# Optimization experiments

Hardware: AMD Instinct MI355X
Metric: run time of the kernel (lower is better)

## Reference

```python
import jax, jax.numpy as jnp
import numpy as np
from jax import lax

NUM_GROUP = 512
GROUP_SIZE = 32
ENC_CH = 384
BN_EPS = 1e-5


def setup_inputs() -> dict:
    key = jax.random.key(0)
    ks = jax.random.split(key, 8)
    B, N = 16, 8192
    def w(k, o, i):
        return jax.random.normal(k, (o, i), jnp.float32) * (1.0 / np.sqrt(i))
    return {
        "xyz": jax.random.normal(ks[0], (B, N, 3), jnp.float32),
        # first_conv: Conv1d(3,128,1)+BN+ReLU, Conv1d(128,256,1)
        "w1": w(ks[1], 128, 3), "b1": jnp.zeros((128,), jnp.float32),
        "g1": jnp.ones((128,), jnp.float32), "bt1": jnp.zeros((128,), jnp.float32),
        "w2": w(ks[2], 256, 128), "b2": jnp.zeros((256,), jnp.float32),
        # second_conv: Conv1d(512,512,1)+BN+ReLU, Conv1d(512,encoder_channel,1)
        "w3": w(ks[3], 512, 512), "b3": jnp.zeros((512,), jnp.float32),
        "g3": jnp.ones((512,), jnp.float32), "bt3": jnp.zeros((512,), jnp.float32),
        "w4": w(ks[4], ENC_CH, 512), "b4": jnp.zeros((ENC_CH,), jnp.float32),
    }


def fps(xyz, npoint):
    """Farthest point sampling. xyz: [B,N,3] -> indices [B,npoint]."""
    B, N, _ = xyz.shape
    def step(carry, _):
        dist, farthest = carry                       # [B,N], [B]
        centroid = jnp.take_along_axis(xyz, farthest[:, None, None], axis=1)  # [B,1,3]
        d = jnp.sum((xyz - centroid) ** 2, axis=-1)  # [B,N]
        dist = jnp.minimum(dist, d)
        nxt = jnp.argmax(dist, axis=-1)
        return (dist, nxt), farthest
    init = (jnp.full((B, N), 1e10, xyz.dtype), jnp.zeros((B,), jnp.int32))
    _, idxs = lax.scan(step, init, None, length=npoint)
    return idxs.T  # [B,npoint]


def knn_point(nsample, xyz, new_xyz):
    """new_xyz [B,S,3], xyz [B,N,3] -> [B,S,nsample] indices of nearest pts."""
    d = (-2.0 * jnp.einsum('bsc,bnc->bsn', new_xyz, xyz)
         + jnp.sum(new_xyz ** 2, -1)[:, :, None]
         + jnp.sum(xyz ** 2, -1)[:, None, :])
    _, idx = lax.top_k(-d, nsample)
    return idx


def batch_norm(x, gamma, beta):
    # x: [M, L, C]; training-mode BN over (M, L) per channel
    mean = jnp.mean(x, axis=(0, 1), keepdims=True)
    var = jnp.var(x, axis=(0, 1), keepdims=True)
    return (x - mean) * lax.rsqrt(var + BN_EPS) * gamma + beta


def reference(xyz, w1, b1, g1, bt1, w2, b2, w3, b3, g3, bt3, w4, b4):
    B, N, _ = xyz.shape
    G, K = NUM_GROUP, GROUP_SIZE
    # ---- Group: FPS centers + kNN neighborhoods, centered ----
    cidx = fps(xyz, G)                                          # [B,G]
    center = jnp.take_along_axis(xyz, cidx[:, :, None], axis=1) # [B,G,3]
    idx = knn_point(K, xyz, center)                             # [B,G,K]
    nb = jnp.take_along_axis(xyz, idx.reshape(B, G * K, 1), axis=1)
    nb = nb.reshape(B, G, K, 3) - center[:, :, None, :]         # [B,G,K,3]
    # ---- Encoder (PointNet stem), 1x1 conv == channel matmul ----
    pg = nb.reshape(B * G, K, 3)                                # [BG,K,3]
    f = jnp.einsum('mkc,oc->mko', pg, w1) + b1                  # [BG,K,128]
    f = jax.nn.relu(batch_norm(f, g1, bt1))
    f = jnp.einsum('mkc,oc->mko', f, w2) + b2                   # [BG,K,256]
    fg = jnp.max(f, axis=1, keepdims=True)                      # [BG,1,256]
    f = jnp.concatenate([jnp.broadcast_to(fg, f.shape), f], axis=-1)  # [BG,K,512]
    f = jnp.einsum('mkc,oc->mko', f, w3) + b3
    f = jax.nn.relu(batch_norm(f, g3, bt3))
    f = jnp.einsum('mkc,oc->mko', f, w4) + b4                   # [BG,K,C]
    feat = jnp.max(f, axis=1)                                   # [BG,C]
    return feat.reshape(B, G, ENC_CH)
```

## Files before the change

### kernel.cpp

```cpp
#include <hip/hip_runtime.h>
#include <cstddef>

#define B_   16
#define N_   8192
#define G_   512
#define K_   32
#define GT   8192
#define NROW 262144
#define EPS  1e-5f

typedef unsigned short ushort_t;
typedef short bf16x8 __attribute__((ext_vector_type(8)));
typedef float f32x4  __attribute__((ext_vector_type(4)));

constexpr size_t OFF_CENTERS = 0;
constexpr size_t OFF_NB      = OFF_CENTERS + 24576;
constexpr size_t OFF_FG      = OFF_NB      + 786432;
constexpr size_t OFF_C1      = OFF_FG      + 2097152;
constexpr size_t OFF_MOM     = OFF_C1      + 1048576;
constexpr size_t OFF_A       = OFF_MOM     + 16;
constexpr size_t OFF_S1      = OFF_A       + 16384;
constexpr size_t OFF_SF      = OFF_S1      + 128;
constexpr size_t OFF_MU      = OFF_SF      + 256;
constexpr size_t OFF_W2S1    = OFF_MU      + 512;
constexpr size_t OFF_BN1A    = OFF_W2S1    + 256;
constexpr size_t OFF_BN1D    = OFF_BN1A    + 128;
constexpr size_t OFF_BN3A    = OFF_BN1D    + 128;
constexpr size_t OFF_BN3D    = OFF_BN3A    + 512;
constexpr size_t OFF_SFF     = OFF_BN3D    + 512;
constexpr size_t OFF_PFCT    = OFF_SFF     + 65536;
constexpr size_t OFF_T1      = OFF_PFCT    + 32768;
constexpr size_t OFF_SCCW    = OFF_T1      + 32768;
constexpr size_t OFF_SFC     = OFF_SCCW    + 65536;
constexpr size_t OFF_W2T     = OFF_SFC     + 65536;
constexpr size_t OFF_W3T     = OFF_W2T     + 32768;
constexpr size_t OFF_W4H     = OFF_W3T     + 262144;
constexpr size_t OFF_W4L     = OFF_W4H     + 98304;
constexpr size_t OFF_APART   = OFF_W4L     + 98304;
constexpr size_t OFF_W23     = OFF_APART   + 8388608;
constexpr size_t OFF_W23H    = OFF_W23     + 65536;
constexpr size_t OFF_W23L    = OFF_W23H    + 32768;
constexpr size_t OFF_W2H     = OFF_W23L    + 32768;
constexpr size_t OFF_W2L     = OFF_W2H     + 16384;
constexpr size_t WS_FLOATS   = OFF_W2L     + 16384;
constexpr size_t OFF_BASE3   = OFF_APART;

__device__ __forceinline__ unsigned bf16_rne(float v) {
    unsigned u = __float_as_uint(v);
    return (u + 0x7fffu + ((u >> 16) & 1u)) >> 16;
}

__global__ __launch_bounds__(1024) void fps_kernel(const float* __restrict__ xyz,
                                                   float* __restrict__ centers) {
    int b = blockIdx.x, t = threadIdx.x;
    const float* xb = xyz + (size_t)b * N_ * 3;
    float px[8], py[8], pz[8], dist[8];
#pragma unroll
    for (int i = 0; i < 8; ++i) {
        int p = t + (i << 10);
        px[i] = xb[p*3]; py[i] = xb[p*3+1]; pz[i] = xb[p*3+2];
        dist[i] = 1e10f;
    }
    __shared__ float redV[2][16];
    __shared__ int   redI[2][16];
    __shared__ float cxyz[2][3];
    if (t == 0) { cxyz[0][0] = px[0]; cxyz[0][1] = py[0]; cxyz[0][2] = pz[0]; }
    __syncthreads();
    for (int it = 0; it < G_; ++it) {
        int cur = it & 1;
        float lcx = cxyz[cur][0], lcy = cxyz[cur][1], lcz = cxyz[cur][2];
        if (t == 0) {
            float* cd = centers + ((size_t)b * G_ + it) * 3;
            cd[0] = lcx; cd[1] = lcy; cd[2] = lcz;
        }
        float bv = -1.0f; int bp = 0;
#pragma unroll
        for (int i = 0; i < 8; ++i) {
            float dx = __fsub_rn(px[i], lcx);
            float dy = __fsub_rn(py[i], lcy);
            float dz = __fsub_rn(pz[i], lcz);
            float d  = __fadd_rn(__fadd_rn(__fmul_rn(dx,dx), __fmul_rn(dy,dy)), __fmul_rn(dz,dz));
            float nd = fminf(dist[i], d);
            dist[i] = nd;
            if (nd > bv) { bv = nd; bp = t + (i << 10); }
        }
#pragma unroll
        for (int off = 1; off < 64; off <<= 1) {
            float ov = __shfl_xor(bv, off);
            int   op = __shfl_xor(bp, off);
            if (ov > bv || (ov == bv && op < bp)) { bv = ov; bp = op; }
        }
        if ((t & 63) == 0) { redV[cur][t >> 6] = bv; redI[cur][t >> 6] = bp; }
        __syncthreads();
        float v = redV[cur][t & 15]; int p = redI[cur][t & 15];
#pragma unroll
        for (int off = 1; off < 16; off <<= 1) {
            float ov = __shfl_xor(v, off);
            int   op = __shfl_xor(p, off);
            if (ov > v || (ov == v && op < p)) { v = ov; p = op; }
        }
        if ((p & 1023) == t) {
            int i = p >> 10;
            cxyz[cur ^ 1][0] = px[i]; cxyz[cur ^ 1][1] = py[i]; cxyz[cur ^ 1][2] = pz[i];
        }
        __syncthreads();
    }
}

__global__ __launch_bounds__(256) void knn_kernel(const float* __restrict__ xyz,
                                                  const float* __restrict__ centers,
                                                  float* __restrict__ nb) {
    int g = blockIdx.x, t = threadIdx.x;
    int b = g >> 9;
    const float* xb = xyz + (size_t)b * N_ * 3;
    const float* c  = centers + (size_t)g * 3;
    float lcx = c[0], lcy = c[1], lcz = c[2];
    float cn2 = __fadd_rn(__fadd_rn(__fmul_rn(lcx,lcx), __fmul_rn(lcy,lcy)), __fmul_rn(lcz,lcz));
    float dreg[32];
    float bvt = 1e30f; int bpt = 0;
#pragma unroll 8
    for (int i = 0; i < 32; ++i) {
        int p = t + (i << 8);
        float x = xb[p*3], y = xb[p*3+1], z = xb[p*3+2];
        float pn2 = __fadd_rn(__fadd_rn(__fmul_rn(x,x), __fmul_rn(y,y)), __fmul_rn(z,z));
        float dot = __fadd_rn(__fadd_rn(__fmul_rn(lcx,x), __fmul_rn(lcy,y)), __fmul_rn(lcz,z));
        float d   = __fadd_rn(__fadd_rn(__fmul_rn(-2.0f,dot), cn2), pn2);
        dreg[i] = d;
        if (d < bvt) { bvt = d; bpt = p; }
    }
    __shared__ float redV[2][4];
    __shared__ int   redI[2][4];
    int myp = 0;
    for (int s = 0; s < K_; ++s) {
        float bv = bvt; int bp = bpt;
#pragma unroll
        for (int off = 1; off < 64; off <<= 1) {
            float ov = __shfl_xor(bv, off);
            int   op = __shfl_xor(bp, off);
            if (ov < bv || (ov == bv && op < bp)) { bv = ov; bp = op; }
        }
        int buf = s & 1;
        if ((t & 63) == 0) { redV[buf][t >> 6] = bv; redI[buf][t >> 6] = bp; }
        __syncthreads();
        float v = redV[buf][0]; int p = redI[buf][0];
#pragma unroll
        for (int w = 1; w < 4; ++w) {
            float ov = redV[buf][w]; int op = redI[buf][w];
            if (ov < v || (ov == v && op < p)) { v = ov; p = op; }
        }
        if (s == t) myp = p;
        if ((p & 255) == t) {
#pragma unroll
            for (int i = 0; i < 32; ++i)
                if (p == t + (i << 8)) dreg[i] = 1e30f;
            bvt = 1e30f; bpt = t;
#pragma unroll
            for (int i = 0; i < 32; ++i) {
                float vv = dreg[i];
                if (vv < bvt) { bvt = vv; bpt = t + (i << 8); }
            }
        }
    }
    if (t < K_) {
        int p = myp;
        float* dst = nb + ((size_t)g * K_ + t) * 3;
        dst[0] = xb[p*3]   - lcx;
        dst[1] = xb[p*3+1] - lcy;
        dst[2] = xb[p*3+2] - lcz;
    }
}

__global__ void zero_mom_kernel(float* __restrict__ mom) {
    if (threadIdx.x < 16) mom[threadIdx.x] = 0.0f;
}

__global__ void moments_kernel(const float* __restrict__ nb, float* __restrict__ mom) {
    int idx = blockIdx.x * 256 + threadIdx.x;
    float x = nb[idx*3], y = nb[idx*3+1], z = nb[idx*3+2];
    float v[9] = {x, y, z, x*x, y*y, z*z, x*y, x*z, y*z};
    __shared__ float red[4][9];
    int t = threadIdx.x;
#pragma unroll
    for (int q = 0; q < 9; ++q) {
        float s = v[q];
#pragma unroll
        for (int off = 32; off; off >>= 1) s += __shfl_xor(s, off);
        if ((t & 63) == 0) red[t >> 6][q] = s;
    }
    __syncthreads();
    if (t < 9) atomicAdd(&mom[t], red[0][t] + red[1][t] + red[2][t] + red[3][t]);
}

__global__ void bn1_params_kernel(const float* __restrict__ mom,
                                  const float* __restrict__ w1, const float* __restrict__ b1,
                                  const float* __restrict__ g1, const float* __restrict__ bt1,
                                  float* __restrict__ bn1a, float* __restrict__ bn1d) {
    int c = threadIdx.x;
    const float inv_n = 1.0f / (float)NROW;
    float mx = mom[0]*inv_n, my = mom[1]*inv_n, mz = mom[2]*inv_n;
    float cxx = mom[3]*inv_n - mx*mx, cyy = mom[4]*inv_n - my*my, czz = mom[5]*inv_n - mz*mz;
    float cxy = mom[6]*inv_n - mx*my, cxz = mom[7]*inv_n - mx*mz, cyz = mom[8]*inv_n - my*mz;
    float wx = w1[c*3], wy = w1[c*3+1], wz = w1[c*3+2];
    float mean = wx*mx + wy*my + wz*mz + b1[c];
    float var  = wx*wx*cxx + wy*wy*cyy + wz*wz*czz
               + 2.0f*(wx*wy*cxy + wx*wz*cxz + wy*wz*cyz);
    float a = rsqrtf(var + EPS) * g1[c];
    bn1a[c] = a;
    bn1d[c] = (b1[c] - mean) * a + bt1[c];
}

__global__ void transpose_kernel(float* __restrict__ out, const float* __restrict__ in, int R, int C) {
    int t = blockIdx.x * blockDim.x + threadIdx.x;
    if (t < R * C) {
        int i = t / C, j = t % C;
        out[(size_t)j * R + i] = in[t];
    }
}

__global__ void split_kernel(const float* __restrict__ src, ushort_t* __restrict__ hi,
                             ushort_t* __restrict__ lo, int n) {
    int i = blockIdx.x * 256 + threadIdx.x;
    if (i < n) {
        float v = src[i];
        unsigned h = bf16_rne(v);
        hi[i] = (ushort_t)h;
        float r = v - __uint_as_float(h << 16);
        lo[i] = (ushort_t)bf16_rne(r);
    }
}

__global__ __launch_bounds__(256) void p1_mfma_kernel(
        const float* __restrict__ nbg, const float* __restrict__ w1,
        const float* __restrict__ bn1a, const float* __restrict__ bn1d,
        const ushort_t* __restrict__ w2h, const ushort_t* __restrict__ w2l,
        const float* __restrict__ b2,
        float* __restrict__ fg, float* __restrict__ c1,
        float* __restrict__ apart) {
    __shared__ short f1h[32*128], f1l[32*128];
    __shared__ short f1Th[128*40], f1Tl[128*40];
    __shared__ float c1part[2][128];
    __shared__ float nbs[96];
    int t = threadIdx.x;
    int lane = t & 63, w = t >> 6;
    int l15 = lane & 15, lh = lane >> 4;

    f32x4 accA[2][8];
#pragma unroll
    for (int i2 = 0; i2 < 2; ++i2)
#pragma unroll
        for (int j = 0; j < 8; ++j) accA[i2][j] = (f32x4){0.f, 0.f, 0.f, 0.f};

    for (int gi = 0; gi < 16; ++gi) {
        int g = blockIdx.x * 16 + gi;
        if (gi == 0 && t < 96) nbs[t] = nbg[(size_t)g * 96 + t];
        __syncthreads();
        {
            int ch = t & 127, rh = t >> 7;
            float a = bn1a[ch], d = bn1d[ch];
            float w0 = w1[ch*3], wa = w1[ch*3+1], wb = w1[ch*3+2];
            float csum = 0.f;
#pragma unroll
            for (int rr = 0; rr < 16; rr += 2) {
                int r0 = rh*16 + rr;
                unsigned hp[2], lp[2];
#pragma unroll
                for (int u = 0; u < 2; ++u) {
                    int r = r0 + u;
                    float x = nbs[r*3], y = nbs[r*3+1], z = nbs[r*3+2];
                    float m = __fmul_rn(x, w0);
                    m = __fmaf_rn(y, wa, m);
                    m = __fmaf_rn(z, wb, m);
                    m = __fmaf_rn(m, a, d);
                    m = fmaxf(m, 0.f);
                    csum = __fadd_rn(csum, m);
                    unsigned h = bf16_rne(m);
                    unsigned l = bf16_rne(m - __uint_as_float(h << 16));
                    hp[u] = h; lp[u] = l;
                    int off = r*256 + ((ch*2) ^ ((r&7)<<4));
                    *(short*)((char*)f1h + off) = (short)h;
                    *(short*)((char*)f1l + off) = (short)l;
                }
                int offT = ch*80 + r0*2;
                *(unsigned*)((char*)f1Th + offT) = hp[0] | (hp[1] << 16);
                *(unsigned*)((char*)f1Tl + offT) = lp[0] | (lp[1] << 16);
            }
            c1part[rh][ch] = csum;
        }
        __syncthreads();
        if (t < 128) c1[(size_t)g*128 + t] = __fadd_rn(c1part[0][t], c1part[1][t]);
        if (gi < 15 && t < 96) nbs[t] = nbg[(size_t)(g+1) * 96 + t];

#pragma unroll
        for (int ci = 0; ci < 4; ++ci) {
            int ct = w*4 + ci;
            f32x4 acc2[2];
            acc2[0] = (f32x4){0.f,0.f,0.f,0.f};
            acc2[1] = (f32x4){0.f,0.f,0.f,0.f};
            __builtin_amdgcn_s_setprio(1);
#pragma unroll
            for (int kq = 0; kq < 4; ++kq) {
                size_t wo = (size_t)(ct*16 + l15)*128 + kq*32 + lh*8;
                bf16x8 wah = *(const bf16x8*)(w2h + wo);
                bf16x8 wal = *(const bf16x8*)(w2l + wo);
#pragma unroll
                for (int pt = 0; pt < 2; ++pt) {
                    int row = pt*16 + l15;
                    int off = row*256 + ((kq*64 + lh*16) ^ ((row&7)<<4));
                    bf16x8 fbh = *(bf16x8*)((char*)f1h + off);
                    bf16x8 fbl = *(bf16x8*)((char*)f1l + off);
                    acc2[pt] = __builtin_amdgcn_mfma_f32_16x16x32_bf16(wah, fbh, acc2[pt], 0, 0, 0);
                    acc2[pt] = __builtin_amdgcn_mfma_f32_16x16x32_bf16(wah, fbl, acc2[pt], 0, 0, 0);
                    acc2[pt] = __builtin_amdgcn_mfma_f32_16x16x32_bf16(wal, fbh, acc2[pt], 0, 0, 0);
                }
            }
            __builtin_amdgcn_s_setprio(0);
            f32x4 mx;
#pragma unroll
            for (int q = 0; q < 4; ++q) mx[q] = fmaxf(acc2[0][q], acc2[1][q]);
#pragma unroll
            for (int off = 1; off < 16; off <<= 1) {
#pragma unroll
                for (int q = 0; q < 4; ++q) mx[q] = fmaxf(mx[q], __shfl_xor(mx[q], off));
            }
            if (l15 == 0) {
                int cb = ct*16 + lh*4;
#pragma unroll
                for (int q = 0; q < 4; ++q)
                    fg[(size_t)g*256 + cb + q] = mx[q] + b2[cb + q];
            }
        }

        {
            bf16x8 ahA[2], alA[2];
#pragma unroll
            for (int i2 = 0; i2 < 2; ++i2) {
                int chi = (2*w + i2)*16 + l15;
                int offA = chi*80 + lh*16;
                ahA[i2] = *(bf16x8*)((char*)f1Th + offA);
                alA[i2] = *(bf16x8*)((char*)f1Tl + offA);
            }
            __builtin_amdgcn_s_setprio(1);
#pragma unroll
            for (int j = 0; j < 8; ++j) {
                int chj = j*16 + l15;
                int offB = chj*80 + lh*16;
                bf16x8 bh = *(bf16x8*)((char*)f1Th + offB);
                bf16x8 bl = *(bf16x8*)((char*)f1Tl + offB);
#pragma unroll
                for (int i2 = 0; i2 < 2; ++i2) {
                    accA[i2][j] = __builtin_amdgcn_mfma_f32_16x16x32_bf16(ahA[i2], bh, accA[i2][j], 0, 0, 0);
                    accA[i2][j] = __builtin_amdgcn_mfma_f32_16x16x32_bf16(ahA[i2], bl, accA[i2][j], 0, 0, 0);
                    accA[i2][j] = __builtin_amdgcn_mfma_f32_16x16x32_bf16(alA[i2], bh, accA[i2][j], 0, 0, 0);
                }
            }
            __builtin_amdgcn_s_setprio(0);
        }
    }
    float* ap = apart + (size_t)blockIdx.x * 16384;
#pragma unroll
    for (int i2 = 0; i2 < 2; ++i2)
#pragma unroll
        for (int j = 0; j < 8; ++j)
#pragma unroll
            for (int q = 0; q < 4; ++q)
                ap[((2*w + i2)*16 + lh*4 + q)*128 + j*16 + l15] = accA[i2][j][q];
}

__global__ void reduce_a_kernel(const float* __restrict__ apart, float* __restrict__ A) {
    int e = blockIdx.x * 256 + threadIdx.x;
    float s = 0.f;
    for (int b = 0; b < 512; ++b) s = __fadd_rn(s, apart[(size_t)b * 16384 + e]);
    A[e] = s;
}

__global__ void reduce_cf_kernel(const float* __restrict__ c1, const float* __restrict__ fgb,
                                 float* __restrict__ s1, float* __restrict__ sf) {
    int c = blockIdx.x, t = threadIdx.x;
    __shared__ float red[256];
    float s = 0.f;
    if (c < 128) { for (int g = t; g < GT; g += 256) s += c1[(size_t)g*128 + c]; }
    else { int cc = c - 128; for (int g = t; g < GT; g += 256) s += fgb[(size_t)g*256 + cc]; }
    red[t] = s; __syncthreads();
    for (int w = 128; w; w >>= 1) { if (t < w) red[t] += red[t + w]; __syncthreads(); }
    if (t == 0) { if (c < 128) s1[c] = red[0]; else sf[c - 128] = red[0]; }
}

__global__ void assemble_mu_kernel(const float* __restrict__ s1, const float* __restrict__ sf,
                                   const float* __restrict__ w2t, const float* __restrict__ b2,
                                   float* __restrict__ mu, float* __restrict__ w2s1) {
    int t = blockIdx.x * 256 + threadIdx.x;
    const float inv_n = 1.0f / (float)NROW;
    if (t < 256) {
        mu[t] = sf[t] * (1.0f / (float)GT);
    } else {
        int c = t - 256;
        float s = 0.f;
        for (int k = 0; k < 128; ++k) s = __fmaf_rn(w2t[k*256 + c], s1[k], s);
        w2s1[c] = s;
        mu[t] = (s + (float)NROW * b2[c]) * inv_n;
    }
}

__global__ __launch_bounds__(256) void gemm_tn_kernel(float* __restrict__ Cm,
                                                      const float* __restrict__ Am, const float* __restrict__ Bm,
                                                      int M, int N, int Kd, int lda, int ldb) {
    __shared__ float As[16][17], Bs[16][17];
    int tx = threadIdx.x & 15, ty = threadIdx.x >> 4;
    int j = blockIdx.x * 16 + tx;
    int i = blockIdx.y * 16 + ty;
    float acc = 0.f;
    for (int k0 = 0; k0 < Kd; k0 += 16) {
        As[ty][tx] = Am[(size_t)(k0 + ty) * lda + blockIdx.y*16 + tx];
        Bs[ty][tx] = Bm[(size_t)(k0 + ty) * ldb + blockIdx.x*16 + tx];
        __syncthreads();
#pragma unroll
        for (int kk = 0; kk < 16; ++kk) acc = __fmaf_rn(As[kk][ty], Bs[kk][tx], acc);
        __syncthreads();
    }
    Cm[(size_t)i * N + j] = acc;
}

__global__ __launch_bounds__(256) void gemm_nn_kernel(float* __restrict__ Cm,
                                                      const float* __restrict__ Am, const float* __restrict__ Bm,
                                                      int M, int N, int Kd, int lda, int ldb) {
    __shared__ float As[16][65], Bs[16][65];
    int t = threadIdx.x;
    int i0 = blockIdx.y * 64, j0 = blockIdx.x * 64;
    int tx = t & 15, ty = t >> 4;
    int lr = t & 63, lk = t >> 6;
    float acc[4][4];
#pragma unroll
    for (int a = 0; a < 4; ++a)
#pragma unroll
        for (int b = 0; b < 4; ++b) acc[a][b] = 0.f;
    for (int k0 = 0; k0 < Kd; k0 += 16) {
#pragma unroll
        for (int u = 0; u < 4; ++u) {
            int k = lk*4 + u;
            As[k][lr] = Am[(size_t)(i0 + lr) * lda + k0 + k];
            Bs[k][lr] = Bm[(size_t)(k0 + k) * ldb + j0 + lr];
        }
        __syncthreads();
#pragma unroll
        for (int kk = 0; kk < 16; ++kk) {
            float av[4], bv[4];
#pragma unroll
            for (int u = 0; u < 4; ++u) av[u] = As[kk][ty*4+u];
#pragma unroll
            for (int u = 0; u < 4; ++u) bv[u] = Bs[kk][tx*4+u];
#pragma unroll
            for (int a = 0; a < 4; ++a)
#pragma unroll
                for (int b = 0; b < 4; ++b) acc[a][b] = __fmaf_rn(av[a], bv[b], acc[a][b]);
        }
        __syncthreads();
    }
#pragma unroll
    for (int a = 0; a < 4; ++a)
#pragma unroll
        for (int b = 0; b < 4; ++b)
            Cm[(size_t)(i0 + ty*4 + a) * N + j0 + tx*4 + b] = acc[a][b];
}

__global__ __launch_bounds__(256) void bn3_params_kernel(const float* __restrict__ w3, const float* __restrict__ b3,
        const float* __restrict__ g3, const float* __restrict__ bt3,
        const float* __restrict__ sff, const float* __restrict__ sfc, const float* __restrict__ sccw,
        const float* __restrict__ sf, const float* __restrict__ w2s1, const float* __restrict__ b2,
        const float* __restrict__ mu, float* __restrict__ bn3a, float* __restrict__ bn3d) {
    int c = blockIdx.x, t = threadIdx.x;
    __shared__ float wL[512];
    __shared__ float red[256];
    wL[t]       = w3[(size_t)c*512 + t];
    wL[256 + t] = w3[(size_t)c*512 + 256 + t];
    __syncthreads();
    float v1 = 0.f, v2 = 0.f, v3 = 0.f;
    for (int i = 0; i < 256; ++i) {
        float wfi = wL[i], wci = wL[256 + i];
        v1 = __fmaf_rn(wfi, sff[(size_t)i*256 + t], v1);
        v2 = __fmaf_rn(wfi, sfc[(size_t)i*256 + t], v2);
        v3 = __fmaf_rn(wci, sccw[(size_t)i*256 + t], v3);
    }
    float wf_t = wL[t], wc_t = wL[256 + t];
    float vals[7];
    vals[0] = v1 * wf_t;
    vals[1] = v2 * wc_t;
    vals[2] = v3 * wc_t;
    vals[3] = wf_t * sf[t];
    vals[4] = wc_t * b2[t];
    vals[5] = wc_t * w2s1[t];
    vals[6] = wf_t * mu[t] + wc_t * mu[256 + t];
    float sums[7];
    for (int q = 0; q < 7; ++q) {
        red[t] = vals[q]; __syncthreads();
        for (int w = 128; w; w >>= 1) { if (t < w) red[t] += red[t + w]; __syncthreads(); }
        sums[q] = red[0]; __syncthreads();
    }
    if (t == 0) {
        float n = (float)NROW;
        float Q = 32.f*sums[0] + 2.f*(sums[1] + 32.f*sums[3]*sums[4])
                + sums[2] + 2.f*sums[5]*sums[4] + n*sums[4]*sums[4];
        float m3 = sums[6] + b3[c];
        float E2 = Q / n + 2.f*b3[c]*sums[6] + b3[c]*b3[c];
        float var = E2 - m3*m3;
        float a = rsqrtf(var + EPS) * g3[c];
        bn3a[c] = a;
        bn3d[c] = (b3[c] + sums[4] - m3) * a + bt3[c];
    }
}

__global__ __launch_bounds__(512) void p3_mfma_kernel(
        const float* __restrict__ nbg, const float* __restrict__ w1,
        const float* __restrict__ bn1a, const float* __restrict__ bn1d,
        const ushort_t* __restrict__ w23h, const ushort_t* __restrict__ w23l,
        const ushort_t* __restrict__ w4h, const ushort_t* __restrict__ w4l,
        const float* __restrict__ base3, const float* __restrict__ bn3a, const float* __restrict__ bn3d,
        const float* __restrict__ b4, float* __restrict__ out) {
    __shared__ short f1h[64*128], f1l[64*128];
    __shared__ short f3h[2][64*64], f3l[2][64*64];
    int t = threadIdx.x;
    int g0 = blockIdx.x * 2;
    {
        int cp = t & 63;
        int r0 = (t >> 6) * 8;
        int c0 = cp * 2;
        const float* nbp = nbg + (size_t)g0 * 96;
        float w00=w1[c0*3+0], w01=w1[c0*3+1], w02=w1[c0*3+2];
        float w10=w1[c0*3+3], w11=w1[c0*3+4], w12=w1[c0*3+5];
        float aA=bn1a[c0], dA=bn1d[c0], aB=bn1a[c0+1], dB=bn1d[c0+1];
#pragma unroll
        for (int rr = 0; rr < 8; ++rr) {
            int r = r0 + rr;
            float x = nbp[r*3], y = nbp[r*3+1], z = nbp[r*3+2];
            float mA = __fmul_rn(x, w00); mA = __fmaf_rn(y, w01, mA); mA = __fmaf_rn(z, w02, mA);
            mA = __fmaf_rn(mA, aA, dA); mA = fmaxf(mA, 0.f);
            float mB = __fmul_rn(x, w10); mB = __fmaf_rn(y, w11, mB); mB = __fmaf_rn(z, w12, mB);
            mB = __fmaf_rn(mB, aB, dB); mB = fmaxf(mB, 0.f);
            unsigned hA = bf16_rne(mA), hB = bf16_rne(mB);
            unsigned lA = bf16_rne(mA - __uint_as_float(hA << 16));
            unsigned lB = bf16_rne(mB - __uint_as_float(hB << 16));
            int off = r*256 + ((cp*4) ^ ((r&7)<<4));
            *(unsigned*)((char*)f1h + off) = hA | (hB << 16);
            *(unsigned*)((char*)f1l + off) = lA | (lB << 16);
        }
    }
    int lane = t & 63, w = t >> 6;
    int l15 = lane & 15, lh = lane >> 4;
    int m3c  = (w & 3) * 16;
    int m3rg = w >> 2;
    int m4g = w >> 2, m4n = (w & 3) * 96;

    f32x4 acc4[2][6];
#pragma unroll
    for (int mt = 0; mt < 2; ++mt)
#pragma unroll
        for (int nt = 0; nt < 6; ++nt) acc4[mt][nt] = (f32x4){0.f, 0.f, 0.f, 0.f};

    const float* b3p = base3 + (size_t)(g0 + m3rg) * 512 + m3c + lh * 4;
    f32x4 b3cur = *(const f32x4*)b3p;
    __syncthreads();

    for (int chunk = 0; chunk < 8; ++chunk) {
        f32x4 b3nxt = b3cur;
        if (chunk < 7) b3nxt = *(const f32x4*)(b3p + (chunk + 1) * 64);
        short* f3hb = &f3h[chunk & 1][0];
        short* f3lb = &f3l[chunk & 1][0];
        f32x4 acc3[2];
        acc3[0] = b3cur; acc3[1] = b3cur;
        __builtin_amdgcn_s_setprio(1);
#pragma unroll
        for (int ks = 0; ks < 4; ++ks) {
            size_t wo = (size_t)(chunk*64 + m3c + l15) * 128 + ks*32 + lh*8;
            bf16x8 wah = *(const bf16x8*)(w23h + wo);
            bf16x8 wal = *(const bf16x8*)(w23l + wo);
#pragma unroll
            for (int nt = 0; nt < 2; ++nt) {
                int row = m3rg*32 + nt*16 + l15;
                int off = row*256 + ((ks*64 + lh*16) ^ ((row&7)<<4));
                bf16x8 fbh = *(bf16x8*)((char*)f1h + off);
                bf16x8 fbl = *(bf16x8*)((char*)f1l + off);
                acc3[nt] = __builtin_amdgcn_mfma_f32_16x16x32_bf16(wah, fbh, acc3[nt], 0, 0, 0);
                acc3[nt] = __builtin_amdgcn_mfma_f32_16x16x32_bf16(wah, fbl, acc3[nt], 0, 0, 0);
                acc3[nt] = __builtin_amdgcn_mfma_f32_16x16x32_bf16(wal, fbh, acc3[nt], 0, 0, 0);
            }
        }
        __builtin_amdgcn_s_setprio(0);
        {
            int cb = chunk*64 + m3c + lh*4;
            f32x4 a4 = *(const f32x4*)(bn3a + cb);
            f32x4 d4 = *(const f32x4*)(bn3d + cb);
#pragma unroll
            for (int nt = 0; nt < 2; ++nt) {
                int row = m3rg*32 + nt*16 + l15;
                unsigned hw0, hw1, lw0, lw1;
                {
                    float v0 = fmaxf(__fmaf_rn(acc3[nt][0], a4[0], d4[0]), 0.f);
                    float v1 = fmaxf(__fmaf_rn(acc3[nt][1], a4[1], d4[1]), 0.f);
                    float v2 = fmaxf(__fmaf_rn(acc3[nt][2], a4[2], d4[2]), 0.f);
                    float v3 = fmaxf(__fmaf_rn(acc3[nt][3], a4[3], d4[3]), 0.f);
                    unsigned h0 = bf16_rne(v0), h1 = bf16_rne(v1), h2 = bf16_rne(v2), h3 = bf16_rne(v3);
                    unsigned l0 = bf16_rne(v0 - __uint_as_float(h0 << 16));
                    unsigned l1 = bf16_rne(v1 - __uint_as_float(h1 << 16));
                    unsigned l2 = bf16_rne(v2 - __uint_as_float(h2 << 16));
                    unsigned l3 = bf16_rne(v3 - __uint_as_float(h3 << 16));
                    hw0 = h0 | (h1 << 16); hw1 = h2 | (h3 << 16);
                    lw0 = l0 | (l1 << 16); lw1 = l2 | (l3 << 16);
                }
                int off = row*128 + (((m3c + lh*4) * 2) ^ ((row&7)<<4));
                *(unsigned long long*)((char*)f3hb + off) = (unsigned long long)hw0 | ((unsigned long long)hw1 << 32);
                *(unsigned long long*)((char*)f3lb + off) = (unsigned long long)lw0 | ((unsigned long long)lw1 << 32);
            }
        }
        __syncthreads();
        __builtin_amdgcn_s_setprio(1);
#pragma unroll
        for (int ks = 0; ks < 2; ++ks) {
            bf16x8 fah[2], fal[2];
#pragma unroll
            for (int mt = 0; mt < 2; ++mt) {
                int row = m4g*32 + mt*16 + l15;
                int off = row*128 + ((ks*64 + lh*16) ^ ((row&7)<<4));
                fah[mt] = *(bf16x8*)((char*)f3hb + off);
                fal[mt] = *(bf16x8*)((char*)f3lb + off);
            }
#pragma unroll
            for (int nt = 0; nt < 6; ++nt) {
                int n = m4n + nt*16 + l15;
                size_t wo = (size_t)n*512 + chunk*64 + ks*32 + lh*8;
                bf16x8 wbh = *(const bf16x8*)(w4h + wo);
                bf16x8 wbl = *(const bf16x8*)(w4l + wo);
#pragma unroll
                for (int mt = 0; mt < 2; ++mt) {
                    acc4[mt][nt] = __builtin_amdgcn_mfma_f32_16x16x32_bf16(fah[mt], wbh, acc4[mt][nt], 0, 0, 0);
                    acc4[mt][nt] = __builtin_amdgcn_mfma_f32_16x16x32_bf16(fah[mt], wbl, acc4[mt][nt], 0, 0, 0);
                    acc4[mt][nt] = __builtin_amdgcn_mfma_f32_16x16x32_bf16(fal[mt], wbh, acc4[mt][nt], 0, 0, 0);
                }
            }
        }
        __builtin_amdgcn_s_setprio(0);
        b3cur = b3nxt;
    }
    int gg = g0 + m4g;
#pragma unroll
    for (int nt = 0; nt < 6; ++nt) {
        int n = m4n + nt*16 + l15;
        float m = acc4[0][nt][0];
#pragma unroll
        for (int q = 1; q < 4; ++q) m = fmaxf(m, acc4[0][nt][q]);
#pragma unroll
        for (int q = 0; q < 4; ++q) m = fmaxf(m, acc4[1][nt][q]);
        m = fmaxf(m, __shfl_xor(m, 16));
        m = fmaxf(m, __shfl_xor(m, 32));
        if (lh == 0) out[(size_t)gg * 384 + n] = m + b4[n];
    }
}

extern "C" void kernel_launch(void* const* d_in, const int* in_sizes, int n_in,
                              void* d_out, int out_size, void* d_ws, size_t ws_size,
                              hipStream_t stream) {
    const float* xyz = (const float*)d_in[0];
    const float* w1  = (const float*)d_in[1];
    const float* b1  = (const float*)d_in[2];
    const float* g1  = (const float*)d_in[3];
    const float* bt1 = (const float*)d_in[4];
    const float* w2  = (const float*)d_in[5];
    const float* b2  = (const float*)d_in[6];
    const float* w3  = (const float*)d_in[7];
    const float* b3  = (const float*)d_in[8];
    const float* g3  = (const float*)d_in[9];
    const float* bt3 = (const float*)d_in[10];
    const float* w4  = (const float*)d_in[11];
    const float* b4  = (const float*)d_in[12];
    float* out = (float*)d_out;
    float* ws  = (float*)d_ws;

    if (ws_size < WS_FLOATS * sizeof(float)) return;

    float* centers = ws + OFF_CENTERS;
    float* nb      = ws + OFF_NB;
    float* fgB     = ws + OFF_FG;
    float* c1B     = ws + OFF_C1;
    float* mom     = ws + OFF_MOM;
    float* A       = ws + OFF_A;
    float* s1      = ws + OFF_S1;
    float* sf      = ws + OFF_SF;
    float* mu      = ws + OFF_MU;
    float* w2s1    = ws + OFF_W2S1;
    float* bn1a    = ws + OFF_BN1A;
    float* bn1d    = ws + OFF_BN1D;
    float* bn3a    = ws + OFF_BN3A;
    float* bn3d    = ws + OFF_BN3D;
    float* sff     = ws + OFF_SFF;
    float* pfct    = ws + OFF_PFCT;
    float* t1m     = ws + OFF_T1;
    float* sccw    = ws + OFF_SCCW;
    float* sfcm    = ws + OFF_SFC;
    float* w2t     = ws + OFF_W2T;
    float* w3t     = ws + OFF_W3T;
    ushort_t* w4h  = (ushort_t*)(ws + OFF_W4H);
    ushort_t* w4l  = (ushort_t*)(ws + OFF_W4L);
    float* apart   = ws + OFF_APART;
    float* w23     = ws + OFF_W23;
    ushort_t* w23h = (ushort_t*)(ws + OFF_W23H);
    ushort_t* w23l = (ushort_t*)(ws + OFF_W23L);
    ushort_t* w2h  = (ushort_t*)(ws + OFF_W2H);
    ushort_t* w2l  = (ushort_t*)(ws + OFF_W2L);
    float* base3   = ws + OFF_BASE3;

    zero_mom_kernel<<<1, 64, 0, stream>>>(mom);
    fps_kernel<<<B_, 1024, 0, stream>>>(xyz, centers);
    knn_kernel<<<GT, 256, 0, stream>>>(xyz, centers, nb);
    moments_kernel<<<NROW/256, 256, 0, stream>>>(nb, mom);
    bn1_params_kernel<<<1, 128, 0, stream>>>(mom, w1, b1, g1, bt1, bn1a, bn1d);
    transpose_kernel<<<(256*128 + 255)/256, 256, 0, stream>>>(w2t, w2, 256, 128);
    transpose_kernel<<<(512*512 + 255)/256, 256, 0, stream>>>(w3t, w3, 512, 512);
    gemm_tn_kernel<<<dim3(8, 32), 256, 0, stream>>>(w23, w3t + 256*512, w2, 512, 128, 256, 512, 128);
    split_kernel<<<(65536 + 255)/256, 256, 0, stream>>>(w23, w23h, w23l, 65536);
    split_kernel<<<(196608 + 255)/256, 256, 0, stream>>>(w4, w4h, w4l, 196608);
    split_kernel<<<(32768 + 255)/256, 256, 0, stream>>>(w2, w2h, w2l, 32768);
    p1_mfma_kernel<<<512, 256, 0, stream>>>(nb, w1, bn1a, bn1d, w2h, w2l, b2, fgB, c1B, apart);
    reduce_a_kernel<<<64, 256, 0, stream>>>(apart, A);
    gemm_nn_kernel<<<dim3(8, 128), 256, 0, stream>>>(base3, fgB, w3t, GT, 512, 256, 256, 512);
    reduce_cf_kernel<<<384, 256, 0, stream>>>(c1B, fgB, s1, sf);
    assemble_mu_kernel<<<2, 256, 0, stream>>>(s1, sf, w2t, b2, mu, w2s1);
    gemm_tn_kernel<<<dim3(16,16), 256, 0, stream>>>(sff,  fgB,  fgB, 256, 256, GT,  256, 256);
    gemm_tn_kernel<<<dim3(16, 8), 256, 0, stream>>>(pfct, c1B,  fgB, 128, 256, GT,  128, 256);
    gemm_tn_kernel<<<dim3(16, 8), 256, 0, stream>>>(t1m,  A,    w2t, 128, 256, 128, 128, 256);
    gemm_tn_kernel<<<dim3(16,16), 256, 0, stream>>>(sccw, w2t,  t1m, 256, 256, 128, 256, 256);
    gemm_tn_kernel<<<dim3(16,16), 256, 0, stream>>>(sfcm, pfct, w2t, 256, 256, 128, 256, 256);
    bn3_params_kernel<<<512, 256, 0, stream>>>(w3, b3, g3, bt3, sff, sfcm, sccw, sf, w2s1, b2, mu, bn3a, bn3d);
    p3_mfma_kernel<<<GT/2, 512, 0, stream>>>(nb, w1, bn1a, bn1d, w23h, w23l, w4h, w4l,
                                             base3, bn3a, bn3d, b4, out);
}
```

Measured before the change: 3.140 ms.

## Retile fused conv3/conv4 MFMA stage with 128-channel chunks and per-wave output columns

Restructures the fused second-conv kernel to process the 512 hidden channels in four 128-wide chunks instead of eight 64-wide double-buffered chunks. Each wave now owns 16 hidden channels across all 64 rows in the first GEMM and 48 output channels across all 64 rows in the second GEMM, so each weight fragment loaded from global memory is reused across four row tiles. This halves the number of chunk iterations and cuts global weight loads per MFMA. In exchange it drops the double-buffered LDS for the intermediate and adds an extra barrier per chunk, and the accumulator layout changes (4x3 tiles).

Result: faster. 2.716 ms (-13.5%).

```diff
diff --git a/kernel.cpp b/kernel.cpp
--- a/kernel.cpp
+++ b/kernel.cpp
@@ -516,7 +516,7 @@
         const float* __restrict__ base3, const float* __restrict__ bn3a, const float* __restrict__ bn3d,
         const float* __restrict__ b4, float* __restrict__ out) {
     __shared__ short f1h[64*128], f1l[64*128];
-    __shared__ short f3h[2][64*64], f3l[2][64*64];
+    __shared__ short f3h[64*128], f3l[64*128];
     int t = threadIdx.x;
     int g0 = blockIdx.x * 2;
     {
@@ -545,58 +545,59 @@
     }
     int lane = t & 63, w = t >> 6;
     int l15 = lane & 15, lh = lane >> 4;
-    int m3c  = (w & 3) * 16;
-    int m3rg = w >> 2;
-    int m4g = w >> 2, m4n = (w & 3) * 96;
-
-    f32x4 acc4[2][6];
-#pragma unroll
-    for (int mt = 0; mt < 2; ++mt)
-#pragma unroll
-        for (int nt = 0; nt < 6; ++nt) acc4[mt][nt] = (f32x4){0.f, 0.f, 0.f, 0.f};
-
-    const float* b3p = base3 + (size_t)(g0 + m3rg) * 512 + m3c + lh * 4;
-    f32x4 b3cur = *(const f32x4*)b3p;
+
+    f32x4 acc4[4][3];
+#pragma unroll
+    for (int mt = 0; mt < 4; ++mt)
+#pragma unroll
+        for (int nt = 0; nt < 3; ++nt) acc4[mt][nt] = (f32x4){0.f, 0.f, 0.f, 0.f};
+
+    const float* b3p0 = base3 + (size_t)g0 * 512 + w*16 + lh*4;
+    const float* b3p1 = base3 + (size_t)(g0 + 1) * 512 + w*16 + lh*4;
+    f32x4 b3c0 = *(const f32x4*)b3p0;
+    f32x4 b3c1 = *(const f32x4*)b3p1;
     __syncthreads();
 
-    for (int chunk = 0; chunk < 8; ++chunk) {
-        f32x4 b3nxt = b3cur;
-        if (chunk < 7) b3nxt = *(const f32x4*)(b3p + (chunk + 1) * 64);
-        short* f3hb = &f3h[chunk & 1][0];
-        short* f3lb = &f3l[chunk & 1][0];
-        f32x4 acc3[2];
-        acc3[0] = b3cur; acc3[1] = b3cur;
+    for (int sc = 0; sc < 4; ++sc) {
+        f32x4 b3n0 = b3c0, b3n1 = b3c1;
+        if (sc < 3) {
+            b3n0 = *(const f32x4*)(b3p0 + (sc + 1) * 128);
+            b3n1 = *(const f32x4*)(b3p1 + (sc + 1) * 128);
+        }
+        f32x4 acc3[4];
+        acc3[0] = b3c0; acc3[1] = b3c0; acc3[2] = b3c1; acc3[3] = b3c1;
         __builtin_amdgcn_s_setprio(1);
 #pragma unroll
         for (int ks = 0; ks < 4; ++ks) {
-            size_t wo = (size_t)(chunk*64 + m3c + l15) * 128 + ks*32 + lh*8;
+            size_t wo = (size_t)(sc*128 + w*16 + l15) * 128 + ks*32 + lh*8;
             bf16x8 wah = *(const bf16x8*)(w23h + wo);
             bf16x8 wal = *(const bf16x8*)(w23l + wo);
 #pragma unroll
-            for (int nt = 0; nt < 2; ++nt) {
-                int row = m3rg*32 + nt*16 + l15;
+            for (int mt = 0; mt < 4; ++mt) {
+                int row = mt*16 + l15;
                 int off = row*256 + ((ks*64 + lh*16) ^ ((row&7)<<4));
                 bf16x8 fbh = *(bf16x8*)((char*)f1h + off);
                 bf16x8 fbl = *(bf16x8*)((char*)f1l + off);
-                acc3[nt] = __builtin_amdgcn_mfma_f32_16x16x32_bf16(wah, fbh, acc3[nt], 0, 0, 0);
-                acc3[nt] = __builtin_amdgcn_mfma_f32_16x16x32_bf16(wah, fbl, acc3[nt], 0, 0, 0);
-                acc3[nt] = __builtin_amdgcn_mfma_f32_16x16x32_bf16(wal, fbh, acc3[nt], 0, 0, 0);
+                acc3[mt] = __builtin_amdgcn_mfma_f32_16x16x32_bf16(wah, fbh, acc3[mt], 0, 0, 0);
+                acc3[mt] = __builtin_amdgcn_mfma_f32_16x16x32_bf16(wah, fbl, acc3[mt], 0, 0, 0);
+                acc3[mt] = __builtin_amdgcn_mfma_f32_16x16x32_bf16(wal, fbh, acc3[mt], 0, 0, 0);
             }
         }
         __builtin_amdgcn_s_setprio(0);
+        __syncthreads();
         {
-            int cb = chunk*64 + m3c + lh*4;
+            int cb = sc*128 + w*16 + lh*4;
             f32x4 a4 = *(const f32x4*)(bn3a + cb);
             f32x4 d4 = *(const f32x4*)(bn3d + cb);
 #pragma unroll
-            for (int nt = 0; nt < 2; ++nt) {
-                int row = m3rg*32 + nt*16 + l15;
+            for (int mt = 0; mt < 4; ++mt) {
+                int row = mt*16 + l15;
                 unsigned hw0, hw1, lw0, lw1;
                 {
-                    float v0 = fmaxf(__fmaf_rn(acc3[nt][0], a4[0], d4[0]), 0.f);
-                    float v1 = fmaxf(__fmaf_rn(acc3[nt][1], a4[1], d4[1]), 0.f);
-                    float v2 = fmaxf(__fmaf_rn(acc3[nt][2], a4[2], d4[2]), 0.f);
-                    float v3 = fmaxf(__fmaf_rn(acc3[nt][3], a4[3], d4[3]), 0.f);
+                    float v0 = fmaxf(__fmaf_rn(acc3[mt][0], a4[0], d4[0]), 0.f);
+                    float v1 = fmaxf(__fmaf_rn(acc3[mt][1], a4[1], d4[1]), 0.f);
+                    float v2 = fmaxf(__fmaf_rn(acc3[mt][2], a4[2], d4[2]), 0.f);
+                    float v3 = fmaxf(__fmaf_rn(acc3[mt][3], a4[3], d4[3]), 0.f);
                     unsigned h0 = bf16_rne(v0), h1 = bf16_rne(v1), h2 = bf16_rne(v2), h3 = bf16_rne(v3);
                     unsigned l0 = bf16_rne(v0 - __uint_as_float(h0 << 16));
                     unsigned l1 = bf16_rne(v1 - __uint_as_float(h1 << 16));
@@ -605,52 +606,57 @@
                     hw0 = h0 | (h1 << 16); hw1 = h2 | (h3 << 16);
                     lw0 = l0 | (l1 << 16); lw1 = l2 | (l3 << 16);
                 }
-                int off = row*128 + (((m3c + lh*4) * 2) ^ ((row&7)<<4));
-                *(unsigned long long*)((char*)f3hb + off) = (unsigned long long)hw0 | ((unsigned long long)hw1 << 32);
-                *(unsigned long long*)((char*)f3lb + off) = (unsigned long long)lw0 | ((unsigned long long)lw1 << 32);
+                int off = row*256 + ((w*32 + lh*8) ^ ((row&7)<<4));
+                *(unsigned long long*)((char*)f3h + off) = (unsigned long long)hw0 | ((unsigned long long)hw1 << 32);
+                *(unsigned long long*)((char*)f3l + off) = (unsigned long long)lw0 | ((unsigned long long)lw1 << 32);
             }
         }
         __syncthreads();
         __builtin_amdgcn_s_setprio(1);
 #pragma unroll
-        for (int ks = 0; ks < 2; ++ks) {
-            bf16x8 fah[2], fal[2];
-#pragma unroll
-            for (int mt = 0; mt < 2; ++mt) {
-                int row = m4g*32 + mt*16 + l15;
-                int off = row*128 + ((ks*64 + lh*16) ^ ((row&7)<<4));
-                fah[mt] = *(bf16x8*)((char*)f3hb + off);
-                fal[mt] = *(bf16x8*)((char*)f3lb + off);
-            }
-#pragma unroll
-            for (int nt = 0; nt < 6; ++nt) {
-                int n = m4n + nt*16 + l15;
-                size_t wo = (size_t)n*512 + chunk*64 + ks*32 + lh*8;
-                bf16x8 wbh = *(const bf16x8*)(w4h + wo);
-                bf16x8 wbl = *(const bf16x8*)(w4l + wo);
-#pragma unroll
-                for (int mt = 0; mt < 2; ++mt) {
-                    acc4[mt][nt] = __builtin_amdgcn_mfma_f32_16x16x32_bf16(fah[mt], wbh, acc4[mt][nt], 0, 0, 0);
-                    acc4[mt][nt] = __builtin_amdgcn_mfma_f32_16x16x32_bf16(fah[mt], wbl, acc4[mt][nt], 0, 0, 0);
-                    acc4[mt][nt] = __builtin_amdgcn_mfma_f32_16x16x32_bf16(fal[mt], wbh, acc4[mt][nt], 0, 0, 0);
+        for (int ks = 0; ks < 4; ++ks) {
+            bf16x8 wbh[3], wbl[3];
+#pragma unroll
+            for (int nt = 0; nt < 3; ++nt) {
+                int n = w*48 + nt*16 + l15;
+                size_t wo = (size_t)n*512 + sc*128 + ks*32 + lh*8;
+                wbh[nt] = *(const bf16x8*)(w4h + wo);
+                wbl[nt] = *(const bf16x8*)(w4l + wo);
+            }
+#pragma unroll
+            for (int mt = 0; mt < 4; ++mt) {
+                int row = mt*16 + l15;
+                int off = row*256 + ((ks*64 + lh*16) ^ ((row&7)<<4));
+                bf16x8 fah = *(bf16x8*)((char*)f3h + off);
+                bf16x8 fal = *(bf16x8*)((char*)f3l + off);
+#pragma unroll
+                for (int nt = 0; nt < 3; ++nt) {
+                    acc4[mt][nt] = __builtin_amdgcn_mfma_f32_16x16x32_bf16(fah, wbh[nt], acc4[mt][nt], 0, 0, 0);
+                    acc4[mt][nt] = __builtin_amdgcn_mfma_f32_16x16x32_bf16(fah, wbl[nt], acc4[mt][nt], 0, 0, 0);
+                    acc4[mt][nt] = __builtin_amdgcn_mfma_f32_16x16x32_bf16(fal, wbh[nt], acc4[mt][nt], 0, 0, 0);
                 }
             }
         }
         __builtin_amdgcn_s_setprio(0);
-        b3cur = b3nxt;
-    }
-    int gg = g0 + m4g;
-#pragma unroll
-    for (int nt = 0; nt < 6; ++nt) {
-        int n = m4n + nt*16 + l15;
-        float m = acc4[0][nt][0];
-#pragma unroll
-        for (int q = 1; q < 4; ++q) m = fmaxf(m, acc4[0][nt][q]);
-#pragma unroll
-        for (int q = 0; q < 4; ++q) m = fmaxf(m, acc4[1][nt][q]);
-        m = fmaxf(m, __shfl_xor(m, 16));
-        m = fmaxf(m, __shfl_xor(m, 32));
-        if (lh == 0) out[(size_t)gg * 384 + n] = m + b4[n];
+        b3c0 = b3n0; b3c1 = b3n1;
+    }
+#pragma unroll
+    for (int nt = 0; nt < 3; ++nt) {
+        int n = w*48 + nt*16 + l15;
+        float m0 = acc4[0][nt][0], m1 = acc4[2][nt][0];
+#pragma unroll
+        for (int q = 1; q < 4; ++q) { m0 = fmaxf(m0, acc4[0][nt][q]); m1 = fmaxf(m1, acc4[2][nt][q]); }
+#pragma unroll
+        for (int q = 0; q < 4; ++q) { m0 = fmaxf(m0, acc4[1][nt][q]); m1 = fmaxf(m1, acc4[3][nt][q]); }
+        m0 = fmaxf(m0, __shfl_xor(m0, 16));
+        m0 = fmaxf(m0, __shfl_xor(m0, 32));
+        m1 = fmaxf(m1, __shfl_xor(m1, 16));
+        m1 = fmaxf(m1, __shfl_xor(m1, 32));
+        if (lh == 0) {
+            float bb = b4[n];
+            out[(size_t)g0 * 384 + n]       = m0 + bb;
+            out[(size_t)(g0 + 1) * 384 + n] = m1 + bb;
+        }
     }
 }
 
```
